# Kernel optimization log

Measured on AMD Instinct MI355X. Metric: run time of the kernel, lower is better.

## Reference

```python
import jax, jax.numpy as jnp
import numpy as np
from jax import lax

B, C, H, W = 8, 64, 128, 128
K = 3           # kernel size
KK = K * K
PAD = K // 2
EPS = 1e-5


def setup_inputs() -> dict:
    key = jax.random.key(0)
    ks = jax.random.split(key, 12)
    s = lambda fan: 1.0 / np.sqrt(fan)
    return {
        "x":      jax.random.normal(ks[0], (B, C, H, W), jnp.float32),
        # offset-predicting conv of the deformable conv: 2*KK offset channels
        "off_w":  jax.random.normal(ks[1], (2 * KK, C, K, K), jnp.float32) * (0.01 * s(C * KK)),
        "off_b":  jnp.zeros((2 * KK,), jnp.float32),
        # deformable conv main weight
        "dw":     jax.random.normal(ks[2], (C, C, K, K), jnp.float32) * s(C * KK),
        "db":     jax.random.normal(ks[3], (C,), jnp.float32) * 0.01,
        # weight_conv1 (1x1)
        "w1":     jax.random.normal(ks[4], (C, C), jnp.float32) * s(C),
        "b1":     jax.random.normal(ks[5], (C,), jnp.float32) * 0.01,
        # BatchNorm (eval mode: running stats)
        "gamma":  jnp.ones((C,), jnp.float32),
        "beta":   jnp.zeros((C,), jnp.float32),
        "rmean":  jax.random.normal(ks[6], (C,), jnp.float32) * 0.01,
        "rvar":   jax.random.uniform(ks[7], (C,), jnp.float32, 0.5, 1.5),
        # weight_conv2 (1x1, downsample=False)
        "w2":     jax.random.normal(ks[8], (C, C), jnp.float32) * s(C),
        "b2":     jax.random.normal(ks[9], (C,), jnp.float32) * 0.01,
    }


def _avg_pool3(x):
    # AvgPool2d(3, stride=1, padding=1), count_include_pad=True (torch default)
    s = lax.reduce_window(x, 0.0, lax.add, (1, 1, 3, 3), (1, 1, 1, 1),
                          [(0, 0), (0, 0), (1, 1), (1, 1)])
    return s / 9.0


def _deform_conv(p, off_w, off_b, dw, db):
    # offsets: [B, 2*KK, H, W] -> [B, KK, 2(y,x), H, W]
    off = lax.conv_general_dilated(p, off_w, (1, 1), [(PAD, PAD), (PAD, PAD)],
                                   dimension_numbers=("NCHW", "OIHW", "NCHW"))
    off = off + off_b[None, :, None, None]
    off = off.reshape(B, KK, 2, H, W)

    # base sampling grid: p0 + pk
    hh = jnp.arange(H, dtype=p.dtype)[:, None]          # [H,1]
    ww = jnp.arange(W, dtype=p.dtype)[None, :]          # [1,W]
    ky = (jnp.arange(KK) // K - PAD).astype(p.dtype)    # [KK]
    kx = (jnp.arange(KK) % K - PAD).astype(p.dtype)
    sy = hh[None, None] + ky[None, :, None, None] + off[:, :, 0]   # [B,KK,H,W]
    sx = ww[None, None] + kx[None, :, None, None] + off[:, :, 1]

    y0 = jnp.floor(sy); x0 = jnp.floor(sx)
    wy = sy - y0;        wx = sx - x0
    y0 = y0.astype(jnp.int32); x0 = x0.astype(jnp.int32)

    pf = p.reshape(B, C, H * W)

    def corner(yc, xc, w):
        valid = ((yc >= 0) & (yc < H) & (xc >= 0) & (xc < W))
        idx = jnp.clip(yc, 0, H - 1) * W + jnp.clip(xc, 0, W - 1)   # [B,KK,H,W]
        g = jax.vmap(lambda f, i: f[:, i])(pf, idx)                  # [B,C,KK,H,W]
        return g * (w * valid.astype(p.dtype))[:, None]

    sampled = (corner(y0,     x0,     (1 - wy) * (1 - wx)) +
               corner(y0,     x0 + 1, (1 - wy) * wx) +
               corner(y0 + 1, x0,     wy * (1 - wx)) +
               corner(y0 + 1, x0 + 1, wy * wx))                      # [B,C,KK,H,W]

    out = jnp.einsum("bckhw,ock->bohw", sampled, dw.reshape(C, C, KK))
    return out + db[None, :, None, None]


def reference(x, off_w, off_b, dw, db, w1, b1, gamma, beta, rmean, rvar, w2, b2):
    p = _avg_pool3(x)
    r = _deform_conv(p, off_w, off_b, dw, db)
    # weight_conv1 (1x1) + BN (eval) + ReLU
    h = jnp.einsum("bchw,oc->bohw", r, w1) + b1[None, :, None, None]
    inv = gamma / jnp.sqrt(rvar + EPS)
    h = h * inv[None, :, None, None] + (beta - rmean * inv)[None, :, None, None]
    h = jax.nn.relu(h)
    h = x + h
    # weight_conv2 (1x1, downsample=False)
    return jnp.einsum("bchw,oc->bohw", h, w2) + b2[None, :, None, None]
```

## Files before the change

### kernel.cpp

```cpp
#include <hip/hip_runtime.h>
#include <hip/hip_bf16.h>
#include <cstddef>

#define H_ 128
#define W_ 128
#define HW_ 16384
#define C_ 64
#define B_ 8
#define EPS_ 1e-5f

#define KSLOTS 19
#define ROWS 616
#define TSTR 72
#define OTSTR 72

typedef __attribute__((ext_vector_type(8))) short bf16x8;
typedef __attribute__((ext_vector_type(4))) float f32x4;

__device__ __forceinline__ unsigned short f2bf(float f) {
  __hip_bfloat16 h = __float2bfloat16(f);
  unsigned short u;
  __builtin_memcpy(&u, &h, 2);
  return u;
}
__device__ __forceinline__ unsigned pack2(float lo, float hi) {
  return (unsigned)f2bf(lo) | ((unsigned)f2bf(hi) << 16);
}
__device__ __forceinline__ float bfl(unsigned short v) {
  return __uint_as_float(((unsigned)v) << 16);
}

__global__ __launch_bounds__(256) void prep_kernel(
    const float* __restrict__ dw, const float* __restrict__ offw,
    const float* __restrict__ w1, const float* __restrict__ b1,
    const float* __restrict__ gamma, const float* __restrict__ beta,
    const float* __restrict__ rmean, const float* __restrict__ rvar,
    const float* __restrict__ w2,
    unsigned short* __restrict__ wf2, unsigned short* __restrict__ offwp,
    unsigned short* __restrict__ w1p, unsigned short* __restrict__ w2p,
    float* __restrict__ b1f) {
  int i = blockIdx.x * 256 + threadIdx.x;
  if (i < 38912) {
    int j = i & 7, l = (i >> 3) & 63, og = (i >> 9) & 3, sg = i >> 11;
    int o = og * 16 + (l & 15);
    int k = sg * 32 + ((l >> 4) << 3) + j;
    int kk = k / 68, c = k - kk * 68;
    float v = (c < 64) ? dw[o * 576 + c * 9 + kk] : 0.f;
    wf2[i] = f2bf(v);
  } else if (i < 38912 + 18432) {
    int j2 = i - 38912;
    int j = j2 & 7, l = (j2 >> 3) & 63, og = (j2 >> 9) & 1, slot = j2 >> 10;
    int kk = slot >> 1, s = slot & 1;
    int oc = og * 16 + (l & 15);
    int c = s * 32 + ((l >> 4) << 3) + j;
    float v = (oc < 18) ? offw[oc * 576 + c * 9 + kk] : 0.f;
    offwp[j2] = f2bf(v);
  } else if (i < 38912 + 18432 + 4096) {
    int j2 = i - 38912 - 18432;
    int j = j2 & 7, l = (j2 >> 3) & 63, og = (j2 >> 9) & 3, sg = j2 >> 11;
    int o = og * 16 + (l & 15);
    int c = sg * 32 + ((l >> 4) << 3) + j;
    float inv = gamma[o] * rsqrtf(rvar[o] + EPS_);
    w1p[j2] = f2bf(w1[o * 64 + c] * inv);
  } else if (i < 38912 + 18432 + 8192) {
    int j2 = i - 38912 - 18432 - 4096;
    int j = j2 & 7, l = (j2 >> 3) & 63, og = (j2 >> 9) & 3, sg = j2 >> 11;
    int o = og * 16 + (l & 15);
    int c = sg * 32 + ((l >> 4) << 3) + j;
    w2p[j2] = f2bf(w2[o * 64 + c]);
  } else if (i < 38912 + 18432 + 8192 + 64) {
    int o = i - 38912 - 18432 - 8192;
    float inv = gamma[o] * rsqrtf(rvar[o] + EPS_);
    b1f[o] = b1[o] * inv + beta[o] - rmean[o] * inv;
  }
}

__global__ __launch_bounds__(256) void avgpool_kernel(const float* __restrict__ xin,
                                                      unsigned short* __restrict__ pbf) {
  __shared__ __align__(16) unsigned short pool[64 * 72];
  int t = threadIdx.x;
  int c = t & 63, wvp = t >> 6;
  int blk = blockIdx.x;
  int half = blk & 1;
  int row = blk >> 1;
  int b = row >> 7, y = row & 127;
  int xb = half * 64 + wvp * 16;
  const float* q = xin + (size_t)(b * C_ + c) * HW_;

  float ver[16];
#pragma unroll
  for (int i = 0; i < 16; ++i) ver[i] = 0.f;
#pragma unroll
  for (int dy = -1; dy <= 1; ++dy) {
    int yy = y + dy;
    if ((unsigned)yy < 128u) {
      const float* r = q + yy * W_;
      float m[18];
      m[0] = (xb > 0) ? r[xb - 1] : 0.f;
      float4 v0 = *(const float4*)(r + xb);
      float4 v1 = *(const float4*)(r + xb + 4);
      float4 v2 = *(const float4*)(r + xb + 8);
      float4 v3 = *(const float4*)(r + xb + 12);
      m[1] = v0.x; m[2] = v0.y; m[3] = v0.z; m[4] = v0.w;
      m[5] = v1.x; m[6] = v1.y; m[7] = v1.z; m[8] = v1.w;
      m[9] = v2.x; m[10] = v2.y; m[11] = v2.z; m[12] = v2.w;
      m[13] = v3.x; m[14] = v3.y; m[15] = v3.z; m[16] = v3.w;
      m[17] = (xb < 112) ? r[xb + 16] : 0.f;
#pragma unroll
      for (int i = 0; i < 16; ++i) ver[i] += m[i] + m[i + 1] + m[i + 2];
    }
  }
  int pxb = wvp * 16;
#pragma unroll
  for (int i = 0; i < 16; ++i) {
    int px = pxb + i;
    int cg = c >> 3;
    pool[px * 72 + ((cg ^ (px & 7)) << 3) + (c & 7)] = f2bf(ver[i] * (1.f / 9.f));
  }
  __syncthreads();

  size_t base = ((size_t)(b * HW_) + y * W_ + half * 64) * 64;
#pragma unroll
  for (int k = 0; k < 2; ++k) {
    int ch = k * 256 + t;
    int px = ch >> 3, g = ch & 7;
    uint2 v = *(const uint2*)(pool + px * 72 + ((g ^ (px & 7)) << 3));
    uint2 v2 = *(const uint2*)(pool + px * 72 + ((g ^ (px & 7)) << 3) + 4);
    *(uint4*)(pbf + base + px * 64 + g * 8) = make_uint4(v.x, v.y, v2.x, v2.y);
  }
}

__global__ __launch_bounds__(256, 4) void offconv_kernel(
    const unsigned short* __restrict__ pbf, const unsigned short* __restrict__ offwp,
    const float* __restrict__ offb, float* __restrict__ off) {
  __shared__ __align__(16) unsigned short tile[198 * OTSTR];
  __shared__ float offT[18 * 64];
  int t = threadIdx.x;
  int lane = t & 63, wv = t >> 6;
  int l15 = lane & 15, lp = lane >> 4;
  int blk = blockIdx.x;
  int half = blk & 1;
  int row = blk >> 1;
  int b = row >> 7, y = row & 127;
  int x0 = half * 64;

#pragma unroll
  for (int it = 0; it < 7; ++it) {
    int ch = it * 256 + t;
    if (ch < 1584) {
      int rc = ch >> 3, g = ch & 7;
      int r = rc / 66, cx = rc - r * 66;
      int iy = y - 1 + r, ix = x0 - 1 + cx;
      uint4 v = make_uint4(0u, 0u, 0u, 0u);
      if (((unsigned)iy < 128u) && ((unsigned)ix < 128u)) {
        v = *(const uint4*)(pbf + ((size_t)(b * HW_) + iy * W_ + ix) * 64 + g * 8);
      }
      *(uint4*)(tile + rc * OTSTR + ((g ^ (rc & 7)) << 3)) = v;
    }
  }
  __syncthreads();

  int og = wv & 1;
  int oc = og * 16 + l15;
  float bo = offb[min(oc, 17)];
  const bf16x8* ofp = (const bf16x8*)offwp;
#pragma unroll
  for (int pti = 0; pti < 2; ++pti) {
    int pt = (wv >> 1) + pti * 2;
    f32x4 aco = (f32x4){bo, bo, bo, bo};
#pragma unroll
    for (int kk = 0; kk < 9; ++kk) {
      int rowb = (kk / 3) * 66 + (kk % 3) + pt * 16 + l15;
#pragma unroll
      for (int s = 0; s < 2; ++s) {
        int ga = s * 4 + lp;
        bf16x8 a = *(const bf16x8*)(tile + rowb * OTSTR + ((ga ^ (rowb & 7)) << 3));
        bf16x8 bw = ofp[((kk * 2 + s) * 2 + og) * 64 + lane];
        aco = __builtin_amdgcn_mfma_f32_16x16x32_bf16(a, bw, aco, 0, 0, 0);
      }
    }
    if (oc < 18) {
#pragma unroll
      for (int j = 0; j < 4; ++j) offT[oc * 64 + pt * 16 + lp * 4 + j] = aco[j];
    }
  }
  __syncthreads();

#pragma unroll
  for (int it = 0; it < 5; ++it) {
    int idx = it * 256 + t;
    if (idx < 1152) {
      int oc2 = idx >> 6, px = idx & 63;
      off[(size_t)(b * 18 + oc2) * HW_ + y * W_ + x0 + px] = offT[idx];
    }
  }
}

__global__ __launch_bounds__(256, 4) void deform_kernel(
    const unsigned short* __restrict__ pbf, const float* __restrict__ off,
    const unsigned short* __restrict__ wf2, const unsigned short* __restrict__ w1p,
    const unsigned short* __restrict__ w2p, const float* __restrict__ db,
    const float* __restrict__ b1f, const float* __restrict__ b2,
    const float* __restrict__ xin, float* __restrict__ out) {
  __shared__ __align__(16) unsigned short tileTb[100 * TSTR];
  __shared__ __align__(16) unsigned short sAb[16 * ROWS];
  __shared__ __align__(16) unsigned short rTb[16 * 72];
  __shared__ __align__(16) unsigned short hTb[16 * 72];
  __shared__ uint2 cwb[144];
  __shared__ uchar4 rel4[144];
  __shared__ int ci4[144];
  __shared__ int wOK[4];
  int t = threadIdx.x;
  int lane = t & 63, wv = t >> 6;
  int l15 = lane & 15, lp = lane >> 4;
  int pix0 = blockIdx.x * 16;
  int b = pix0 >> 14;
  int yx0 = pix0 & 16383;
  int y = yx0 >> 7, x0 = yx0 & 127;
  int ty = min(max(y - 2, 0), 123);
  int tx = min(max(x0 - 2, 0), 108);
  const unsigned short* pB = pbf + (size_t)(b * HW_) * 64;

  int o_me = wv * 16 + l15;
  int px0 = lp * 4;
  const float4 xv = *(const float4*)(xin + (size_t)(b * C_ + o_me) * HW_ + yx0 + px0);

  bool ok = true;
  int pixl = t & 15, kk = t >> 4;
  bool active = (t < 144);
  if (active) {
    int xx = x0 + pixl;
    const float* ob = off + (size_t)(b * 18 + kk * 2) * HW_ + y * W_ + xx;
    float offy = ob[0];
    float offx = ob[HW_];
    float sy = (float)(y + (kk / 3) - 1) + offy;
    float sx = (float)(xx + (kk % 3) - 1) + offx;
    float fy = floorf(sy), fx = floorf(sx);
    float wy = sy - fy, wx = sx - fx;
    int iy = (int)fy, ix = (int)fx;
    float w[4];
    int rc[4];
    int id0 = 0;
#pragma unroll
    for (int j = 0; j < 4; ++j) {
      int dy = j >> 1, dx = j & 1;
      int yc = iy + dy, xc = ix + dx;
      bool v = ((unsigned)yc < 128u) && ((unsigned)xc < 128u);
      int ycc = min(max(yc, 0), 127), xcc = min(max(xc, 0), 127);
      float wgt = (dy ? wy : 1.f - wy) * (dx ? wx : 1.f - wx);
      w[j] = v ? wgt : 0.f;
      if (j == 0) id0 = ycc * W_ + xcc;
      bool in_tile = (ycc >= ty) && (ycc <= ty + 4) && (xcc >= tx) && (xcc <= tx + 19);
      ok = ok && ((w[j] == 0.f) || in_tile);
      int ry = min(max(ycc - ty, 0), 4);
      int rx = min(max(xcc - tx, 0), 19);
      rc[j] = ry * 20 + rx;
    }
    cwb[t] = make_uint2(pack2(w[0], w[1]), pack2(w[2], w[3]));
    rel4[t] = make_uchar4((unsigned char)rc[0], (unsigned char)rc[1],
                          (unsigned char)rc[2], (unsigned char)rc[3]);
    ci4[t] = id0;
    *(uint2*)(sAb + pixl * ROWS + kk * 68 + 64) = make_uint2(0u, 0u);
  }
  {
    unsigned long long m = __ballot(ok);
    if (lane == 0) wOK[wv] = (m == ~0ull) ? 1 : 0;
  }

#pragma unroll
  for (int it = 0; it < 3; ++it) {
    int ch = it * 256 + t;
    int rc = ch >> 3, g = ch & 7;
    int r = rc / 20, cx = rc - r * 20;
    uint4 v = *(const uint4*)(pB + ((size_t)((ty + r) * W_ + tx + cx)) * 64 + g * 8);
    *(uint4*)(tileTb + rc * TSTR + ((g ^ (rc & 7)) << 3)) = v;
  }
  if (t < 32) {
    int ch = 768 + t;
    int rc = ch >> 3, g = ch & 7;
    int r = rc / 20, cx = rc - r * 20;
    uint4 v = *(const uint4*)(pB + ((size_t)((ty + r) * W_ + tx + cx)) * 64 + g * 8);
    *(uint4*)(tileTb + rc * TSTR + ((g ^ (rc & 7)) << 3)) = v;
  }
  __syncthreads();

  bool fast = wOK[0] && wOK[1] && wOK[2] && wOK[3];

  if (fast) {
    auto do_slot = [&](int slot) {
      int job = slot >> 1, hf = slot & 1;
      int jp = job & 15, jk = job >> 4;
      int bg = hf * 4;
      uint2 wp = cwb[job];
      float w0 = bfl((unsigned short)(wp.x & 0xffffu));
      float w1_ = bfl((unsigned short)(wp.x >> 16));
      float w2_ = bfl((unsigned short)(wp.y & 0xffffu));
      float w3_ = bfl((unsigned short)(wp.y >> 16));
      uchar4 rl = rel4[job];
      int r0 = rl.x, r1 = rl.y, r2 = rl.z, r3 = rl.w;
      unsigned short* wr = sAb + jp * ROWS + jk * 68 + hf * 32;
#pragma unroll
      for (int gg = 0; gg < 4; ++gg) {
        int g = bg + gg;
        bf16x8 v0 = *(const bf16x8*)(tileTb + r0 * TSTR + ((g ^ (r0 & 7)) << 3));
        bf16x8 v1 = *(const bf16x8*)(tileTb + r1 * TSTR + ((g ^ (r1 & 7)) << 3));
        bf16x8 v2 = *(const bf16x8*)(tileTb + r2 * TSTR + ((g ^ (r2 & 7)) << 3));
        bf16x8 v3 = *(const bf16x8*)(tileTb + r3 * TSTR + ((g ^ (r3 & 7)) << 3));
        unsigned dws[4];
#pragma unroll
        for (int e = 0; e < 8; e += 2) {
          float lo = w0 * bfl((unsigned short)v0[e]) + w1_ * bfl((unsigned short)v1[e]) +
                     w2_ * bfl((unsigned short)v2[e]) + w3_ * bfl((unsigned short)v3[e]);
          float hi = w0 * bfl((unsigned short)v0[e + 1]) + w1_ * bfl((unsigned short)v1[e + 1]) +
                     w2_ * bfl((unsigned short)v2[e + 1]) + w3_ * bfl((unsigned short)v3[e + 1]);
          dws[e >> 1] = pack2(lo, hi);
        }
        *(uint2*)(wr + gg * 8) = make_uint2(dws[0], dws[1]);
        *(uint2*)(wr + gg * 8 + 4) = make_uint2(dws[2], dws[3]);
      }
    };
    do_slot(t);
    if ((t & 7) == 0) do_slot(256 + (t >> 3));
  } else {
    if (active) {
      int xx = x0 + pixl;
      const float* ob = off + (size_t)(b * 18 + kk * 2) * HW_ + y * W_ + xx;
      float offy = ob[0];
      float offx = ob[HW_];
      float sy = (float)(y + (kk / 3) - 1) + offy;
      float sx = (float)(xx + (kk % 3) - 1) + offx;
      float fy = floorf(sy), fx = floorf(sx);
      float wy = sy - fy, wx = sx - fx;
      int iy = (int)fy, ix = (int)fx;
      float wj[4];
      const unsigned short* pc[4];
#pragma unroll
      for (int j = 0; j < 4; ++j) {
        int dy = j >> 1, dx = j & 1;
        int yc = iy + dy, xc = ix + dx;
        bool v = ((unsigned)yc < 128u) && ((unsigned)xc < 128u);
        int ycc = min(max(yc, 0), 127), xcc = min(max(xc, 0), 127);
        wj[j] = v ? (dy ? wy : 1.f - wy) * (dx ? wx : 1.f - wx) : 0.f;
        pc[j] = pB + ((size_t)(ycc * W_ + xcc)) * 64;
      }
      unsigned short* wr = sAb + pixl * ROWS + kk * 68;
#pragma unroll 4
      for (int c = 0; c < 64; ++c) {
        float v = wj[0] * bfl(pc[0][c]) + wj[1] * bfl(pc[1][c]) +
                  wj[2] * bfl(pc[2][c]) + wj[3] * bfl(pc[3][c]);
        wr[c] = f2bf(v);
      }
    }
  }
  __syncthreads();

  f32x4 acc;
  {
    float d = db[o_me];
    acc = (f32x4){d, d, d, d};
  }
  const unsigned short* arow = sAb + l15 * ROWS + (lp << 3);
  const bf16x8* wfp = (const bf16x8*)wf2;
#pragma unroll
  for (int s = 0; s < KSLOTS; ++s) {
    bf16x8 a = *(const bf16x8*)(arow + s * 32);
    bf16x8 bw = wfp[(s * 4 + wv) * 64 + lane];
    acc = __builtin_amdgcn_mfma_f32_16x16x32_bf16(a, bw, acc, 0, 0, 0);
  }

#pragma unroll
  for (int j = 0; j < 4; ++j) {
    rTb[(px0 + j) * 72 + o_me] = f2bf(acc[j]);
  }
  __syncthreads();

  f32x4 acc1;
  {
    float bb = b1f[o_me];
    acc1 = (f32x4){bb, bb, bb, bb};
  }
  const unsigned short* arow1 = rTb + l15 * 72 + (lp << 3);
  const bf16x8* w1f8 = (const bf16x8*)w1p;
#pragma unroll
  for (int s = 0; s < 2; ++s) {
    bf16x8 a = *(const bf16x8*)(arow1 + s * 32);
    bf16x8 bw = w1f8[(s * 4 + wv) * 64 + lane];
    acc1 = __builtin_amdgcn_mfma_f32_16x16x32_bf16(a, bw, acc1, 0, 0, 0);
  }
  float h0 = fmaxf(acc1[0], 0.f) + xv.x;
  float h1 = fmaxf(acc1[1], 0.f) + xv.y;
  float h2 = fmaxf(acc1[2], 0.f) + xv.z;
  float h3 = fmaxf(acc1[3], 0.f) + xv.w;
  hTb[(px0 + 0) * 72 + o_me] = f2bf(h0);
  hTb[(px0 + 1) * 72 + o_me] = f2bf(h1);
  hTb[(px0 + 2) * 72 + o_me] = f2bf(h2);
  hTb[(px0 + 3) * 72 + o_me] = f2bf(h3);
  __syncthreads();

  f32x4 acc2;
  {
    float bo = b2[o_me];
    acc2 = (f32x4){bo, bo, bo, bo};
  }
  const unsigned short* arow2 = hTb + l15 * 72 + (lp << 3);
  const bf16x8* w2f8 = (const bf16x8*)w2p;
#pragma unroll
  for (int s = 0; s < 2; ++s) {
    bf16x8 a = *(const bf16x8*)(arow2 + s * 32);
    bf16x8 bw = w2f8[(s * 4 + wv) * 64 + lane];
    acc2 = __builtin_amdgcn_mfma_f32_16x16x32_bf16(a, bw, acc2, 0, 0, 0);
  }
  *(float4*)(out + (size_t)(b * C_ + o_me) * HW_ + yx0 + px0) =
      make_float4(acc2[0], acc2[1], acc2[2], acc2[3]);
}

extern "C" void kernel_launch(void* const* d_in, const int* in_sizes, int n_in,
                              void* d_out, int out_size, void* d_ws, size_t ws_size,
                              hipStream_t stream) {
  const float* x = (const float*)d_in[0];
  const float* offw = (const float*)d_in[1];
  const float* offb = (const float*)d_in[2];
  const float* dw = (const float*)d_in[3];
  const float* db = (const float*)d_in[4];
  const float* w1 = (const float*)d_in[5];
  const float* b1 = (const float*)d_in[6];
  const float* gamma = (const float*)d_in[7];
  const float* beta = (const float*)d_in[8];
  const float* rmean = (const float*)d_in[9];
  const float* rvar = (const float*)d_in[10];
  const float* w2 = (const float*)d_in[11];
  const float* b2 = (const float*)d_in[12];
  float* out = (float*)d_out;

  unsigned short* pbf = (unsigned short*)d_ws;
  float* off = (float*)(pbf + 8388608);
  unsigned short* wf2 = (unsigned short*)(off + 2359296);
  unsigned short* offwp = wf2 + 38912;
  unsigned short* w1p = offwp + 18432;
  unsigned short* w2p = w1p + 4096;
  float* b1f = (float*)(w2p + 4096);

  prep_kernel<<<257, 256, 0, stream>>>(dw, offw, w1, b1, gamma, beta, rmean,
                                       rvar, w2, wf2, offwp, w1p, w2p, b1f);
  avgpool_kernel<<<2048, 256, 0, stream>>>(x, pbf);
  offconv_kernel<<<2048, 256, 0, stream>>>(pbf, offwp, offb, off);
  deform_kernel<<<8192, 256, 0, stream>>>(pbf, off, wf2, w1p, w2p, db, b1f, b2,
                                          x, out);
}
```

Baseline: 118.0 us.

## Fuse offset-predicting conv into deform kernel using the shared pooled tile

Drops the separate offconv kernel and computes the 18 offset channels for each 16-pixel block inside the deform kernel with MFMA. It reads the pooled tile already staged in shared memory and splits the K dimension across wave pairs, reducing through a new shared buffer. The tile is now zero-padded at borders instead of clamped. This removes the offset buffer's global write and read and one kernel launch. In exchange it adds MFMA work and shared memory per block, and occupancy is lowered to 3 blocks per SIMD in launch bounds.

Result: slower. 123.7 us (+4.8%).

```diff
diff --git a/kernel.cpp b/kernel.cpp
--- a/kernel.cpp
+++ b/kernel.cpp
@@ -12,7 +12,6 @@
 #define KSLOTS 19
 #define ROWS 616
 #define TSTR 72
-#define OTSTR 72
 
 typedef __attribute__((ext_vector_type(8))) short bf16x8;
 typedef __attribute__((ext_vector_type(4))) float f32x4;
@@ -130,85 +129,20 @@
   }
 }
 
-__global__ __launch_bounds__(256, 4) void offconv_kernel(
-    const unsigned short* __restrict__ pbf, const unsigned short* __restrict__ offwp,
-    const float* __restrict__ offb, float* __restrict__ off) {
-  __shared__ __align__(16) unsigned short tile[198 * OTSTR];
-  __shared__ float offT[18 * 64];
-  int t = threadIdx.x;
-  int lane = t & 63, wv = t >> 6;
-  int l15 = lane & 15, lp = lane >> 4;
-  int blk = blockIdx.x;
-  int half = blk & 1;
-  int row = blk >> 1;
-  int b = row >> 7, y = row & 127;
-  int x0 = half * 64;
-
-#pragma unroll
-  for (int it = 0; it < 7; ++it) {
-    int ch = it * 256 + t;
-    if (ch < 1584) {
-      int rc = ch >> 3, g = ch & 7;
-      int r = rc / 66, cx = rc - r * 66;
-      int iy = y - 1 + r, ix = x0 - 1 + cx;
-      uint4 v = make_uint4(0u, 0u, 0u, 0u);
-      if (((unsigned)iy < 128u) && ((unsigned)ix < 128u)) {
-        v = *(const uint4*)(pbf + ((size_t)(b * HW_) + iy * W_ + ix) * 64 + g * 8);
-      }
-      *(uint4*)(tile + rc * OTSTR + ((g ^ (rc & 7)) << 3)) = v;
-    }
-  }
-  __syncthreads();
-
-  int og = wv & 1;
-  int oc = og * 16 + l15;
-  float bo = offb[min(oc, 17)];
-  const bf16x8* ofp = (const bf16x8*)offwp;
-#pragma unroll
-  for (int pti = 0; pti < 2; ++pti) {
-    int pt = (wv >> 1) + pti * 2;
-    f32x4 aco = (f32x4){bo, bo, bo, bo};
-#pragma unroll
-    for (int kk = 0; kk < 9; ++kk) {
-      int rowb = (kk / 3) * 66 + (kk % 3) + pt * 16 + l15;
-#pragma unroll
-      for (int s = 0; s < 2; ++s) {
-        int ga = s * 4 + lp;
-        bf16x8 a = *(const bf16x8*)(tile + rowb * OTSTR + ((ga ^ (rowb & 7)) << 3));
-        bf16x8 bw = ofp[((kk * 2 + s) * 2 + og) * 64 + lane];
-        aco = __builtin_amdgcn_mfma_f32_16x16x32_bf16(a, bw, aco, 0, 0, 0);
-      }
-    }
-    if (oc < 18) {
-#pragma unroll
-      for (int j = 0; j < 4; ++j) offT[oc * 64 + pt * 16 + lp * 4 + j] = aco[j];
-    }
-  }
-  __syncthreads();
-
-#pragma unroll
-  for (int it = 0; it < 5; ++it) {
-    int idx = it * 256 + t;
-    if (idx < 1152) {
-      int oc2 = idx >> 6, px = idx & 63;
-      off[(size_t)(b * 18 + oc2) * HW_ + y * W_ + x0 + px] = offT[idx];
-    }
-  }
-}
-
-__global__ __launch_bounds__(256, 4) void deform_kernel(
-    const unsigned short* __restrict__ pbf, const float* __restrict__ off,
-    const unsigned short* __restrict__ wf2, const unsigned short* __restrict__ w1p,
-    const unsigned short* __restrict__ w2p, const float* __restrict__ db,
+__global__ __launch_bounds__(256, 3) void deform_kernel(
+    const unsigned short* __restrict__ pbf,
+    const unsigned short* __restrict__ wf2, const unsigned short* __restrict__ offwp,
+    const unsigned short* __restrict__ w1p, const unsigned short* __restrict__ w2p,
+    const float* __restrict__ offb, const float* __restrict__ db,
     const float* __restrict__ b1f, const float* __restrict__ b2,
     const float* __restrict__ xin, float* __restrict__ out) {
   __shared__ __align__(16) unsigned short tileTb[100 * TSTR];
   __shared__ __align__(16) unsigned short sAb[16 * ROWS];
+  __shared__ __align__(16) float redO[4 * 64 * 4];
   __shared__ __align__(16) unsigned short rTb[16 * 72];
   __shared__ __align__(16) unsigned short hTb[16 * 72];
   __shared__ uint2 cwb[144];
   __shared__ uchar4 rel4[144];
-  __shared__ int ci4[144];
   __shared__ int wOK[4];
   int t = threadIdx.x;
   int lane = t & 63, wv = t >> 6;
@@ -217,22 +151,69 @@
   int b = pix0 >> 14;
   int yx0 = pix0 & 16383;
   int y = yx0 >> 7, x0 = yx0 & 127;
-  int ty = min(max(y - 2, 0), 123);
-  int tx = min(max(x0 - 2, 0), 108);
+  int ty = y - 2, tx = x0 - 2;
   const unsigned short* pB = pbf + (size_t)(b * HW_) * 64;
 
   int o_me = wv * 16 + l15;
   int px0 = lp * 4;
   const float4 xv = *(const float4*)(xin + (size_t)(b * C_ + o_me) * HW_ + yx0 + px0);
 
+#pragma unroll
+  for (int it = 0; it < 3; ++it) {
+    int ch = it * 256 + t;
+    int rc = ch >> 3, g = ch & 7;
+    int r = rc / 20, cx = rc - r * 20;
+    int iy = ty + r, ix = tx + cx;
+    uint4 v = make_uint4(0u, 0u, 0u, 0u);
+    if (((unsigned)iy < 128u) && ((unsigned)ix < 128u)) {
+      v = *(const uint4*)(pB + ((size_t)(iy * W_ + ix)) * 64 + g * 8);
+    }
+    *(uint4*)(tileTb + rc * TSTR + ((g ^ (rc & 7)) << 3)) = v;
+  }
+  if (t < 32) {
+    int ch = 768 + t;
+    int rc = ch >> 3, g = ch & 7;
+    int r = rc / 20, cx = rc - r * 20;
+    int iy = ty + r, ix = tx + cx;
+    uint4 v = make_uint4(0u, 0u, 0u, 0u);
+    if (((unsigned)iy < 128u) && ((unsigned)ix < 128u)) {
+      v = *(const uint4*)(pB + ((size_t)(iy * W_ + ix)) * 64 + g * 8);
+    }
+    *(uint4*)(tileTb + rc * TSTR + ((g ^ (rc & 7)) << 3)) = v;
+  }
+  __syncthreads();
+
+  {
+    int og = wv & 1, shalf = wv >> 1;
+    f32x4 aco = (f32x4){0.f, 0.f, 0.f, 0.f};
+    const bf16x8* ofp = (const bf16x8*)offwp;
+#pragma unroll
+    for (int si = 0; si < 9; ++si) {
+      int slot = shalf * 9 + si;
+      int kk = slot >> 1, s = slot & 1;
+      int rc = (1 + kk / 3) * 20 + (1 + (kk % 3)) + l15;
+      int ga = s * 4 + lp;
+      bf16x8 a = *(const bf16x8*)(tileTb + rc * TSTR + ((ga ^ (rc & 7)) << 3));
+      bf16x8 bw = ofp[(slot * 2 + og) * 64 + lane];
+      aco = __builtin_amdgcn_mfma_f32_16x16x32_bf16(a, bw, aco, 0, 0, 0);
+    }
+    *(f32x4*)&redO[(wv * 64 + lane) * 4] = aco;
+  }
+  __syncthreads();
+
   bool ok = true;
+  float offy = 0.f, offx = 0.f;
   int pixl = t & 15, kk = t >> 4;
   bool active = (t < 144);
   if (active) {
+    int ocy = 2 * kk, ocx = ocy + 1;
+    int ogy = ocy >> 4, ogx = ocx >> 4;
+    int lny = ((pixl >> 2) << 4) | (ocy & 15);
+    int lnx = ((pixl >> 2) << 4) | (ocx & 15);
+    int jj = pixl & 3;
+    offy = redO[(ogy * 64 + lny) * 4 + jj] + redO[((ogy + 2) * 64 + lny) * 4 + jj] + offb[ocy];
+    offx = redO[(ogx * 64 + lnx) * 4 + jj] + redO[((ogx + 2) * 64 + lnx) * 4 + jj] + offb[ocx];
     int xx = x0 + pixl;
-    const float* ob = off + (size_t)(b * 18 + kk * 2) * HW_ + y * W_ + xx;
-    float offy = ob[0];
-    float offx = ob[HW_];
     float sy = (float)(y + (kk / 3) - 1) + offy;
     float sx = (float)(xx + (kk % 3) - 1) + offx;
     float fy = floorf(sy), fx = floorf(sx);
@@ -240,7 +221,6 @@
     int iy = (int)fy, ix = (int)fx;
     float w[4];
     int rc[4];
-    int id0 = 0;
 #pragma unroll
     for (int j = 0; j < 4; ++j) {
       int dy = j >> 1, dx = j & 1;
@@ -249,7 +229,6 @@
       int ycc = min(max(yc, 0), 127), xcc = min(max(xc, 0), 127);
       float wgt = (dy ? wy : 1.f - wy) * (dx ? wx : 1.f - wx);
       w[j] = v ? wgt : 0.f;
-      if (j == 0) id0 = ycc * W_ + xcc;
       bool in_tile = (ycc >= ty) && (ycc <= ty + 4) && (xcc >= tx) && (xcc <= tx + 19);
       ok = ok && ((w[j] == 0.f) || in_tile);
       int ry = min(max(ycc - ty, 0), 4);
@@ -259,28 +238,11 @@
     cwb[t] = make_uint2(pack2(w[0], w[1]), pack2(w[2], w[3]));
     rel4[t] = make_uchar4((unsigned char)rc[0], (unsigned char)rc[1],
                           (unsigned char)rc[2], (unsigned char)rc[3]);
-    ci4[t] = id0;
     *(uint2*)(sAb + pixl * ROWS + kk * 68 + 64) = make_uint2(0u, 0u);
   }
   {
     unsigned long long m = __ballot(ok);
     if (lane == 0) wOK[wv] = (m == ~0ull) ? 1 : 0;
-  }
-
-#pragma unroll
-  for (int it = 0; it < 3; ++it) {
-    int ch = it * 256 + t;
-    int rc = ch >> 3, g = ch & 7;
-    int r = rc / 20, cx = rc - r * 20;
-    uint4 v = *(const uint4*)(pB + ((size_t)((ty + r) * W_ + tx + cx)) * 64 + g * 8);
-    *(uint4*)(tileTb + rc * TSTR + ((g ^ (rc & 7)) << 3)) = v;
-  }
-  if (t < 32) {
-    int ch = 768 + t;
-    int rc = ch >> 3, g = ch & 7;
-    int r = rc / 20, cx = rc - r * 20;
-    uint4 v = *(const uint4*)(pB + ((size_t)((ty + r) * W_ + tx + cx)) * 64 + g * 8);
-    *(uint4*)(tileTb + rc * TSTR + ((g ^ (rc & 7)) << 3)) = v;
   }
   __syncthreads();
 
@@ -324,9 +286,6 @@
   } else {
     if (active) {
       int xx = x0 + pixl;
-      const float* ob = off + (size_t)(b * 18 + kk * 2) * HW_ + y * W_ + xx;
-      float offy = ob[0];
-      float offx = ob[HW_];
       float sy = (float)(y + (kk / 3) - 1) + offy;
       float sx = (float)(xx + (kk % 3) - 1) + offx;
       float fy = floorf(sy), fx = floorf(sx);
@@ -433,8 +392,7 @@
   float* out = (float*)d_out;
 
   unsigned short* pbf = (unsigned short*)d_ws;
-  float* off = (float*)(pbf + 8388608);
-  unsigned short* wf2 = (unsigned short*)(off + 2359296);
+  unsigned short* wf2 = pbf + 8388608;
   unsigned short* offwp = wf2 + 38912;
   unsigned short* w1p = offwp + 18432;
   unsigned short* w2p = w1p + 4096;
@@ -443,7 +401,6 @@
   prep_kernel<<<257, 256, 0, stream>>>(dw, offw, w1, b1, gamma, beta, rmean,
                                        rvar, w2, wf2, offwp, w1p, w2p, b1f);
   avgpool_kernel<<<2048, 256, 0, stream>>>(x, pbf);
-  offconv_kernel<<<2048, 256, 0, stream>>>(pbf, offwp, offb, off);
-  deform_kernel<<<8192, 256, 0, stream>>>(pbf, off, wf2, w1p, w2p, db, b1f, b2,
-                                          x, out);
-}
+  deform_kernel<<<8192, 256, 0, stream>>>(pbf, wf2, offwp, w1p, w2p, offb, db,
+                                          b1f, b2, x, out);
+}
```
